# Performance work log

Measured on AMD Instinct MI355X. Metric: run time of the kernel, lower is better.

## Reference

```python
import jax, jax.numpy as jnp
import numpy as np

CELL = 4  # 2 ** cell_2_pow, cell_2_pow = 2
EPS = 1e-5


def conv2d(x, w, b):
    # 3x3 conv, padding 1, NCHW / OIHW
    y = jax.lax.conv_general_dilated(
        x, w, window_strides=(1, 1), padding=((1, 1), (1, 1)),
        dimension_numbers=('NCHW', 'OIHW', 'NCHW'))
    return y + b[None, :, None, None]


def setup_inputs() -> dict:
    key = jax.random.key(0)
    ks = jax.random.split(key, 4)
    B, Cc, H, W = 8, 128, 512, 512
    nh, nw = H // CELL, W // CELL  # ctrl spatial must be padded_img / cell_sz
    return dict(
        image_pipe=jax.random.normal(ks[0], (B, 6, H, W), jnp.float32),
        ctrl_pipe=jax.random.normal(ks[1], (B, Cc, nh, nw), jnp.float32),
        w1=jax.random.normal(ks[2], (50, Cc, 3, 3), jnp.float32) * 0.03,
        b1=jnp.zeros((50,), jnp.float32),
        gamma=jnp.ones((50,), jnp.float32),
        beta=jnp.zeros((50,), jnp.float32),
        mean=jnp.zeros((50,), jnp.float32),
        var=jnp.ones((50,), jnp.float32),
        w2=jax.random.normal(ks[3], (18, 50, 3, 3), jnp.float32) * 0.05,
        b2=jnp.zeros((18,), jnp.float32),
    )


def reference(image_pipe, ctrl_pipe, w1, b1, gamma, beta, mean, var, w2, b2):
    cs = CELL
    B, C6, H, W = image_pipe.shape
    # conv_condense: Conv(Cc->50) -> ReLU -> BatchNorm2d(50, inference) -> Conv(50->18)
    h = jax.nn.relu(conv2d(ctrl_pipe, w1, b1))
    scale = gamma * jax.lax.rsqrt(var + EPS)
    h = (h - mean[None, :, None, None]) * scale[None, :, None, None] + beta[None, :, None, None]
    cond = conv2d(h, w2, b2)  # [B, 18, nh, nw]
    nh, nw = cond.shape[-2], cond.shape[-1]

    padH = (-H) % cs
    padW = (-W) % cs
    rH, rW = H + padH, W + padW
    # F.pad(img, (cell, padW+cell, cell, padH+cell)): left/right then top/bottom
    img = jnp.pad(image_pipe, ((0, 0), (0, 0), (cs, padH + cs), (cs, padW + cs)))

    # 9 cell-strided shifted views; torch loop order: i over width (outer), j over height (inner)
    stack = jnp.stack(
        [img[:, :, j * cs:j * cs + rH, i * cs:i * cs + rW]
         for i in range(3) for j in range(3)], axis=-1)  # [B, 6, rH, rW, 9]
    stack = stack.reshape(B, 2, 3, rH, rW, 9)  # 2 groups of 3 channels

    # per-pixel dynamic 9-tap weights, constant within each cs x cs cell
    wts = cond.reshape(B, 2, 9, nh, nw)
    wts = jnp.repeat(jnp.repeat(wts, cs, axis=3), cs, axis=4)  # [B, 2, 9, rH, rW]

    out = jnp.einsum('bgchwk,bgkhw->bgchw', stack, wts)  # weighted neighborhood sum
    out = out.reshape(B, 6, rH, rW)[:, :, :H, :W]
    return out
```

## Files before the change

kernel.cpp:

```cpp
#include <hip/hip_runtime.h>

typedef __attribute__((ext_vector_type(8))) short short8;
typedef __attribute__((ext_vector_type(4))) float floatx4;

__device__ __forceinline__ unsigned short f2bf(float f) {
    union { float f; unsigned int u; } v; v.f = f;
    unsigned int r = (v.u + 0x7fffu + ((v.u >> 16) & 1u)) >> 16;
    return (unsigned short)r;
}

__device__ __forceinline__ void gload_lds16(const void* g, void* l) {
    __builtin_amdgcn_global_load_lds(
        (const __attribute__((address_space(1))) unsigned int*)g,
        (__attribute__((address_space(3))) unsigned int*)l, 16, 0, 0);
}

__global__ __launch_bounds__(256) void prep_w_kernel(
    const float* __restrict__ w1, const float* __restrict__ w2,
    unsigned short* __restrict__ w1p, unsigned short* __restrict__ w2p,
    unsigned short* __restrict__ hbuf)
{
    int i = blockIdx.x * 256 + threadIdx.x;
    if (i < 73728) {
        int ci = i & 31; int t2 = i >> 5; int co = t2 & 63; int t3 = t2 >> 6;
        int tap = t3 % 9; int c4 = t3 / 9;
        float v = 0.f;
        if (co < 50) v = w1[((size_t)co * 128 + c4 * 32 + ci) * 9 + tap];
        w1p[i] = f2bf(v);
    } else if (i < 92160) {
        int j = i - 73728;
        int ci = j & 31; int t2 = j >> 5; int co = t2 & 31; int t3 = t2 >> 5;
        int tap = t3 % 9; int c4 = t3 / 9;
        int cig = c4 * 32 + ci;
        float v = 0.f;
        if (co < 18 && cig < 50) v = w2[((size_t)co * 50 + cig) * 9 + tap];
        w2p[j] = f2bf(v);
    } else {
        int k = i - 92160;
        int b = k / 4128, r = k % 4128;
        int px = r >> 3, u4 = r & 7;
        int Y, X;
        if (px < 130)      { Y = 0;        X = px; }
        else if (px < 260) { Y = 129;      X = px - 130; }
        else if (px < 388) { Y = px - 259; X = 0; }
        else               { Y = px - 387; X = 129; }
        *(uint4*)&hbuf[(((size_t)b * 130 + Y) * 130 + X) * 64 + u4 * 8] = make_uint4(0, 0, 0, 0);
    }
}

__global__ __launch_bounds__(256, 2) void conv1_mfma(
    const float* __restrict__ ctrl, const unsigned short* __restrict__ w1p,
    const float* __restrict__ b1, const float* __restrict__ gamma,
    const float* __restrict__ beta, const float* __restrict__ mean,
    const float* __restrict__ var, unsigned short* __restrict__ h)
{
    __shared__ unsigned short in_s[324 * 32];
    __shared__ unsigned short w_s[2304 * 8];
    const int tid = threadIdx.x;
    const int x0 = blockIdx.x * 16, y0 = blockIdx.y * 16, b = blockIdx.z;
    const int wid = tid >> 6, lane = tid & 63;
    const int ln = lane & 15, q = lane >> 4;

    floatx4 acc[4][4];
#pragma unroll
    for (int mt = 0; mt < 4; mt++)
#pragma unroll
        for (int nt = 0; nt < 4; nt++) acc[mt][nt] = (floatx4)(0.f);

    for (int c4 = 0; c4 < 4; c4++) {
        const unsigned short* wsrc = &w1p[(size_t)c4 * 2304 * 8];
#pragma unroll
        for (int it = 0; it < 9; it++) {
            const int cbase = it * 256 + wid * 64;
            gload_lds16(&wsrc[(size_t)(cbase + lane) * 8], &w_s[(size_t)cbase * 8]);
        }
#pragma unroll
        for (int r = 0; r < 3; r++) {
            const int i = r * 256 + tid;
            const bool ok = i < 576;
            const int row = i >> 5, ci = i & 31;
            const int gy = y0 - 1 + row;
            float4 wv[6];
#pragma unroll
            for (int f = 0; f < 6; f++) {
                const int xs = x0 - 4 + f * 4;
                wv[f] = make_float4(0.f, 0.f, 0.f, 0.f);
                if (ok && gy >= 0 && gy < 128 && xs >= 0 && xs < 125)
                    wv[f] = *(const float4*)&ctrl[(((size_t)b * 128 + c4 * 32 + ci) * 128 + gy) * 128 + xs];
            }
            if (ok) {
                float va[24];
#pragma unroll
                for (int f = 0; f < 6; f++) {
                    va[4 * f + 0] = wv[f].x; va[4 * f + 1] = wv[f].y;
                    va[4 * f + 2] = wv[f].z; va[4 * f + 3] = wv[f].w;
                }
                unsigned short* dst = &in_s[(row * 18) * 32 + ci];
#pragma unroll
                for (int k = 0; k < 18; k++)
                    dst[k * 32] = f2bf(va[k + 3]);
            }
        }
        __syncthreads();

#pragma unroll
        for (int tap = 0; tap < 9; tap++) {
            const int dy = tap / 3, dx = tap % 3;
            short8 a[4];
#pragma unroll
            for (int mt = 0; mt < 4; mt++)
                a[mt] = *(const short8*)&in_s[((wid * 4 + mt + dy) * 18 + ln + dx) * 32 + q * 8];
#pragma unroll
            for (int nt = 0; nt < 4; nt++) {
                short8 bf = *(const short8*)&w_s[((tap * 64 + nt * 16 + ln) * 4 + q) * 8];
#pragma unroll
                for (int mt = 0; mt < 4; mt++)
                    acc[mt][nt] = __builtin_amdgcn_mfma_f32_16x16x32_bf16(a[mt], bf, acc[mt][nt], 0, 0, 0);
            }
        }
        __syncthreads();
    }

#pragma unroll
    for (int nt = 0; nt < 4; nt++) {
        int co = nt * 16 + ln;
        bool real = co < 50;
        float sc = 0.f, mn = 0.f, bt = 0.f, bs = 0.f;
        if (real) {
            sc = gamma[co] * rsqrtf(var[co] + 1e-5f);
            mn = mean[co]; bt = beta[co]; bs = b1[co];
        }
#pragma unroll
        for (int mt = 0; mt < 4; mt++) {
            int gy = y0 + wid * 4 + mt;
#pragma unroll
            for (int r = 0; r < 4; r++) {
                int px = q * 4 + r;
                float v = 0.f;
                if (real) {
                    float tv = fmaxf(acc[mt][nt][r] + bs, 0.f);
                    v = (tv - mn) * sc + bt;
                }
                h[(((size_t)b * 130 + (gy + 1)) * 130 + (x0 + px + 1)) * 64 + co] = f2bf(v);
            }
        }
    }
}

__global__ __launch_bounds__(256) void conv2_mfma(
    const unsigned short* __restrict__ hT, const unsigned short* __restrict__ w2p,
    const float* __restrict__ b2, float* __restrict__ cond)
{
    __shared__ unsigned short in_s[1344 * 8];
    __shared__ unsigned short w_s[1152 * 8];
    const int tid = threadIdx.x;
    const int x0 = blockIdx.x * 16, y0 = blockIdx.y * 16, b = blockIdx.z;
    const int wid = tid >> 6, lane = tid & 63;
    const int ln = lane & 15, q = lane >> 4;

    floatx4 acc[4][2];
#pragma unroll
    for (int mt = 0; mt < 4; mt++)
#pragma unroll
        for (int nt = 0; nt < 2; nt++) acc[mt][nt] = (floatx4)(0.f);

    for (int c4 = 0; c4 < 2; c4++) {
#pragma unroll
        for (int it = 0; it < 6; it++) {
            const int cbase = it * 256 + wid * 64;
            if (cbase < 1296) {
                int j = cbase + lane; if (j > 1295) j = 1295;
                const int p = j >> 2, s = j & 3;
                const int Y = y0 + p / 18, X = x0 + p % 18;
                gload_lds16(&hT[(((size_t)b * 130 + Y) * 130 + X) * 64 + c4 * 32 + s * 8],
                            &in_s[(size_t)cbase * 8]);
            }
        }
        const unsigned short* wsrc = &w2p[(size_t)c4 * 1152 * 8];
#pragma unroll
        for (int it = 0; it < 5; it++) {
            const int cbase = it * 256 + wid * 64;
            if (cbase < 1152)
                gload_lds16(&wsrc[(size_t)(cbase + lane) * 8], &w_s[(size_t)cbase * 8]);
        }
        __syncthreads();

#pragma unroll
        for (int tap = 0; tap < 9; tap++) {
            const int dy = tap / 3, dx = tap % 3;
            short8 a[4];
#pragma unroll
            for (int mt = 0; mt < 4; mt++)
                a[mt] = *(const short8*)&in_s[(((wid * 4 + mt + dy) * 18 + ln + dx) * 4 + q) * 8];
#pragma unroll
            for (int nt = 0; nt < 2; nt++) {
                short8 bf = *(const short8*)&w_s[((tap * 32 + nt * 16 + ln) * 4 + q) * 8];
#pragma unroll
                for (int mt = 0; mt < 4; mt++)
                    acc[mt][nt] = __builtin_amdgcn_mfma_f32_16x16x32_bf16(a[mt], bf, acc[mt][nt], 0, 0, 0);
            }
        }
        __syncthreads();
    }

#pragma unroll
    for (int nt = 0; nt < 2; nt++) {
        int co = nt * 16 + ln;
        if (co < 18) {
            float bs = b2[co];
            int gch = co / 9, k = co % 9;
            int iw = k / 3, jy = k % 3;
#pragma unroll
            for (int mt = 0; mt < 4; mt++) {
                int gy = y0 + wid * 4 + mt;
#pragma unroll
                for (int r = 0; r < 4; r++) {
                    int px = q * 4 + r;
                    cond[((((size_t)b * 2 + gch) * 128 + gy) * 128 + (x0 + px)) * 12 + jy * 4 + iw]
                        = acc[mt][nt][r] + bs;
                }
            }
        }
    }
}

__global__ __launch_bounds__(256) void apply_kernel(
    const float* __restrict__ img, const float* __restrict__ cond,
    float* __restrict__ out)
{
    const int hwid = blockIdx.x;
    const int lid = (hwid & 7) * 512 + (hwid >> 3);
    const int bx = lid & 1, by = (lid >> 1) & 127, bz = lid >> 8;

    const int tid = threadIdx.x;
    const int xl = tid & 63, s = tid >> 6;
    const int x4 = bx * 64 + xl;
    const int o = by * 4 + s;
    const int b = bz >> 1, g = bz & 1;
    const int xo = x4 * 4;

    const float* cw = &cond[((((size_t)b * 2 + g) * 128 + by) * 128 + x4) * 12];
    float4 w0 = *(const float4*)&cw[0];
    float4 w1 = *(const float4*)&cw[4];
    float4 w2 = *(const float4*)&cw[8];

    float4 C[3][3], L[3][3], R[3][3];
    const bool lok = (x4 > 0), rok_x = (x4 < 127);
#pragma unroll
    for (int jy = 0; jy < 3; jy++) {
        const int r = o - 4 + 4 * jy;
        const bool rk = (r >= 0) && (r < 512);
#pragma unroll
        for (int cc = 0; cc < 3; cc++) {
            C[jy][cc] = make_float4(0.f, 0.f, 0.f, 0.f);
            L[jy][cc] = make_float4(0.f, 0.f, 0.f, 0.f);
            R[jy][cc] = make_float4(0.f, 0.f, 0.f, 0.f);
            if (rk) {
                const float* rp = &img[((((size_t)b * 6 + g * 3 + cc) * 512) + r) * 512];
                C[jy][cc] = *(const float4*)&rp[xo];
                if (lok)   L[jy][cc] = *(const float4*)&rp[xo - 4];
                if (rok_x) R[jy][cc] = *(const float4*)&rp[xo + 4];
            }
        }
    }

    float4 acc[3];
#pragma unroll
    for (int cc = 0; cc < 3; cc++) acc[cc] = make_float4(0.f, 0.f, 0.f, 0.f);

#pragma unroll
    for (int jy = 0; jy < 3; jy++) {
        const float4 wj = (jy == 0) ? w0 : (jy == 1) ? w1 : w2;
#pragma unroll
        for (int cc = 0; cc < 3; cc++) {
            const float4 l = L[jy][cc], c = C[jy][cc], r = R[jy][cc];
            acc[cc].x += l.x * wj.x + c.x * wj.y + r.x * wj.z;
            acc[cc].y += l.y * wj.x + c.y * wj.y + r.y * wj.z;
            acc[cc].z += l.z * wj.x + c.z * wj.y + r.z * wj.z;
            acc[cc].w += l.w * wj.x + c.w * wj.y + r.w * wj.z;
        }
    }

#pragma unroll
    for (int cc = 0; cc < 3; cc++)
        *(float4*)&out[((((size_t)b * 6 + g * 3 + cc) * 512) + o) * 512 + xo] = acc[cc];
}

extern "C" void kernel_launch(void* const* d_in, const int* in_sizes, int n_in,
                              void* d_out, int out_size, void* d_ws, size_t ws_size,
                              hipStream_t stream)
{
    const float* img   = (const float*)d_in[0];
    const float* ctrl  = (const float*)d_in[1];
    const float* w1    = (const float*)d_in[2];
    const float* b1    = (const float*)d_in[3];
    const float* gamma = (const float*)d_in[4];
    const float* beta  = (const float*)d_in[5];
    const float* mean  = (const float*)d_in[6];
    const float* var   = (const float*)d_in[7];
    const float* w2    = (const float*)d_in[8];
    const float* b2    = (const float*)d_in[9];
    float* out = (float*)d_out;

    char* ws = (char*)d_ws;
    unsigned short* hbuf  = (unsigned short*)ws;
    float*          cond  = (float*)(ws + 17305600);
    unsigned short* w1p   = (unsigned short*)(ws + 29888512);
    unsigned short* w2p   = (unsigned short*)(ws + 30035968);

    prep_w_kernel<<<489, 256, 0, stream>>>(w1, w2, w1p, w2p, hbuf);
    conv1_mfma<<<dim3(8, 8, 8), 256, 0, stream>>>(ctrl, w1p, b1, gamma, beta, mean, var, hbuf);
    conv2_mfma<<<dim3(8, 8, 8), 256, 0, stream>>>(hbuf, w2p, b2, cond);
    apply_kernel<<<4096, 256, 0, stream>>>(img, cond, out);
}
```

Before: 224.7 us.

## Fuse conv2 with dynamic-filter apply stage into a single kernel

The apply stage is merged into the conv2 kernel: after computing its 16x16 tile of cond weights and writing them to global memory, each block syncs and applies the 9-tap filter to the 64x64 image pixels covered by that tile, for both channel groups. This removes one kernel launch and lets the cond tile be re-read while still in cache. The cost is that apply parallelism drops from 4096 blocks to 512 blocks, each doing 8 sequential row-group iterations, which may reduce memory-level parallelism for the bandwidth-bound image pass. It relies on __syncthreads plus global memory visibility within the block for the cond values.

```diff
diff --git a/kernel.cpp b/kernel.cpp
--- a/kernel.cpp
+++ b/kernel.cpp
@@ -147,9 +147,10 @@
     }
 }
 
-__global__ __launch_bounds__(256) void conv2_mfma(
+__global__ __launch_bounds__(256) void conv2_apply(
     const unsigned short* __restrict__ hT, const unsigned short* __restrict__ w2p,
-    const float* __restrict__ b2, float* __restrict__ cond)
+    const float* __restrict__ b2, float* __restrict__ cond,
+    const float* __restrict__ img, float* __restrict__ out)
 {
     __shared__ unsigned short in_s[1344 * 8];
     __shared__ unsigned short w_s[1152 * 8];
@@ -222,68 +223,65 @@
             }
         }
     }
-}
-
-__global__ __launch_bounds__(256) void apply_kernel(
-    const float* __restrict__ img, const float* __restrict__ cond,
-    float* __restrict__ out)
-{
-    const int hwid = blockIdx.x;
-    const int lid = (hwid & 7) * 512 + (hwid >> 3);
-    const int bx = lid & 1, by = (lid >> 1) & 127, bz = lid >> 8;
-
-    const int tid = threadIdx.x;
-    const int xl = tid & 63, s = tid >> 6;
-    const int x4 = bx * 64 + xl;
-    const int o = by * 4 + s;
-    const int b = bz >> 1, g = bz & 1;
-    const int xo = x4 * 4;
-
-    const float* cw = &cond[((((size_t)b * 2 + g) * 128 + by) * 128 + x4) * 12];
-    float4 w0 = *(const float4*)&cw[0];
-    float4 w1 = *(const float4*)&cw[4];
-    float4 w2 = *(const float4*)&cw[8];
-
-    float4 C[3][3], L[3][3], R[3][3];
-    const bool lok = (x4 > 0), rok_x = (x4 < 127);
-#pragma unroll
-    for (int jy = 0; jy < 3; jy++) {
-        const int r = o - 4 + 4 * jy;
-        const bool rk = (r >= 0) && (r < 512);
-#pragma unroll
-        for (int cc = 0; cc < 3; cc++) {
-            C[jy][cc] = make_float4(0.f, 0.f, 0.f, 0.f);
-            L[jy][cc] = make_float4(0.f, 0.f, 0.f, 0.f);
-            R[jy][cc] = make_float4(0.f, 0.f, 0.f, 0.f);
-            if (rk) {
-                const float* rp = &img[((((size_t)b * 6 + g * 3 + cc) * 512) + r) * 512];
-                C[jy][cc] = *(const float4*)&rp[xo];
-                if (lok)   L[jy][cc] = *(const float4*)&rp[xo - 4];
-                if (rok_x) R[jy][cc] = *(const float4*)&rp[xo + 4];
-            }
-        }
-    }
-
-    float4 acc[3];
-#pragma unroll
-    for (int cc = 0; cc < 3; cc++) acc[cc] = make_float4(0.f, 0.f, 0.f, 0.f);
-
-#pragma unroll
-    for (int jy = 0; jy < 3; jy++) {
-        const float4 wj = (jy == 0) ? w0 : (jy == 1) ? w1 : w2;
-#pragma unroll
-        for (int cc = 0; cc < 3; cc++) {
-            const float4 l = L[jy][cc], c = C[jy][cc], r = R[jy][cc];
-            acc[cc].x += l.x * wj.x + c.x * wj.y + r.x * wj.z;
-            acc[cc].y += l.y * wj.x + c.y * wj.y + r.y * wj.z;
-            acc[cc].z += l.z * wj.x + c.z * wj.y + r.z * wj.z;
-            acc[cc].w += l.w * wj.x + c.w * wj.y + r.w * wj.z;
-        }
-    }
-
-#pragma unroll
-    for (int cc = 0; cc < 3; cc++)
-        *(float4*)&out[((((size_t)b * 6 + g * 3 + cc) * 512) + o) * 512 + xo] = acc[cc];
+
+    __syncthreads();
+
+    {
+        const int xl = tid & 15, sr = tid >> 4;
+        const int x4 = x0 + xl;
+        const int xo = x4 * 4;
+        const bool lok = (x4 > 0), rokx = (x4 < 127);
+#pragma unroll
+        for (int rr = 0; rr < 4; rr++) {
+            const int o = (y0 << 2) + rr * 16 + sr;
+            const int cy = o >> 2;
+#pragma unroll
+            for (int g = 0; g < 2; g++) {
+                const float* cw = &cond[((((size_t)b * 2 + g) * 128 + cy) * 128 + x4) * 12];
+                const float4 w0 = *(const float4*)&cw[0];
+                const float4 w1 = *(const float4*)&cw[4];
+                const float4 w2v = *(const float4*)&cw[8];
+
+                float4 C[3][3], L[3][3], R[3][3];
+#pragma unroll
+                for (int jy = 0; jy < 3; jy++) {
+                    const int r = o - 4 + 4 * jy;
+                    const bool rk = (r >= 0) && (r < 512);
+#pragma unroll
+                    for (int cc = 0; cc < 3; cc++) {
+                        C[jy][cc] = make_float4(0.f, 0.f, 0.f, 0.f);
+                        L[jy][cc] = make_float4(0.f, 0.f, 0.f, 0.f);
+                        R[jy][cc] = make_float4(0.f, 0.f, 0.f, 0.f);
+                        if (rk) {
+                            const float* rp = &img[((((size_t)b * 6 + g * 3 + cc) * 512) + r) * 512];
+                            C[jy][cc] = *(const float4*)&rp[xo];
+                            if (lok)  L[jy][cc] = *(const float4*)&rp[xo - 4];
+                            if (rokx) R[jy][cc] = *(const float4*)&rp[xo + 4];
+                        }
+                    }
+                }
+
+                float4 a2[3];
+#pragma unroll
+                for (int cc = 0; cc < 3; cc++) a2[cc] = make_float4(0.f, 0.f, 0.f, 0.f);
+#pragma unroll
+                for (int jy = 0; jy < 3; jy++) {
+                    const float4 wj = (jy == 0) ? w0 : (jy == 1) ? w1 : w2v;
+#pragma unroll
+                    for (int cc = 0; cc < 3; cc++) {
+                        const float4 l = L[jy][cc], c = C[jy][cc], r = R[jy][cc];
+                        a2[cc].x += l.x * wj.x + c.x * wj.y + r.x * wj.z;
+                        a2[cc].y += l.y * wj.x + c.y * wj.y + r.y * wj.z;
+                        a2[cc].z += l.z * wj.x + c.z * wj.y + r.z * wj.z;
+                        a2[cc].w += l.w * wj.x + c.w * wj.y + r.w * wj.z;
+                    }
+                }
+#pragma unroll
+                for (int cc = 0; cc < 3; cc++)
+                    *(float4*)&out[((((size_t)b * 6 + g * 3 + cc) * 512) + o) * 512 + xo] = a2[cc];
+            }
+        }
+    }
 }
 
 extern "C" void kernel_launch(void* const* d_in, const int* in_sizes, int n_in,
@@ -310,6 +308,5 @@
 
     prep_w_kernel<<<489, 256, 0, stream>>>(w1, w2, w1p, w2p, hbuf);
     conv1_mfma<<<dim3(8, 8, 8), 256, 0, stream>>>(ctrl, w1p, b1, gamma, beta, mean, var, hbuf);
-    conv2_mfma<<<dim3(8, 8, 8), 256, 0, stream>>>(hbuf, w2p, b2, cond);
-    apply_kernel<<<4096, 256, 0, stream>>>(img, cond, out);
-}
+    conv2_apply<<<dim3(8, 8, 8), 256, 0, stream>>>(hbuf, w2p, b2, cond, img, out);
+}
```

After: 245.0 us. +9.0%, slower.
